# Performance work log

Measured on AMD Instinct MI355X. Metric: run time of the kernel, lower is better.

The kernel has to match this reference:

```python
import jax, jax.numpy as jnp
import numpy as np

N_E, E_DIM = 2048, 256
B, H, W = 32, 32, 32


def setup_inputs() -> dict:
    key = jax.random.key(0)
    k1, k2 = jax.random.split(key)
    z = jax.random.normal(k1, (B, E_DIM, H, W), dtype=jnp.float32)
    embedding = jax.random.normal(k2, (N_E, E_DIM), dtype=jnp.float32)
    return {"z": z, "embedding": embedding}


def reference(z, embedding):
    # z: [B, C, H, W] with C == e_dim; embedding: [n_e, e_dim]
    n_e, e_dim = embedding.shape
    b, c, h, w = z.shape
    z_nhwc = jnp.transpose(z, (0, 2, 3, 1))            # [B,H,W,C]
    z_flat = z_nhwc.reshape(-1, e_dim)                 # [L, D]
    # squared euclidean distance: ||z||^2 + ||e||^2 - 2 z.e^T
    d = (
        jnp.sum(z_flat * z_flat, axis=1, keepdims=True)
        + jnp.sum(embedding * embedding, axis=1)
        - 2.0 * jnp.einsum("ld,nd->ln", z_flat, embedding)
    )                                                  # [L, n_e]
    idx = jnp.argmin(d, axis=1)                        # [L]
    z_q = jnp.take(embedding, idx, axis=0).reshape(b, h, w, e_dim)
    # embed_ema=True -> commitment-only loss (codebook updated by EMA, not grads)
    loss = jnp.mean((jax.lax.stop_gradient(z_q) - z_nhwc) ** 2)
    # straight-through estimator
    z_q_st = z_nhwc + jax.lax.stop_gradient(z_q - z_nhwc)
    quantize = jnp.transpose(z_q_st, (0, 3, 1, 2))     # [B,C,H,W]
    # number of distinct codebook entries used (jit-safe via scatter-set)
    used = jnp.sum(jnp.zeros((n_e,), z.dtype).at[idx].set(1.0))
    index = idx.reshape(b, h, w)
    return quantize, loss, index, used
```

## Files before the change

### kernel.cpp

```cpp
#include <hip/hip_runtime.h>
#include <cfloat>

#define Dm 256
#define HW 1024
#define NE 2048
#define L_TOT 32768
#define QOFF 8388608
#define TAU 0.02f

typedef __attribute__((ext_vector_type(8))) short bf16x8;
typedef __attribute__((ext_vector_type(4))) float f32x4;
typedef const __attribute__((address_space(1))) unsigned int* as1_u32p;
typedef __attribute__((address_space(3))) unsigned int* as3_u32p;

#define GLL(gp, lp) __builtin_amdgcn_global_load_lds((as1_u32p)(gp), (as3_u32p)(lp), 16, 0, 0)

__device__ __forceinline__ unsigned short f2bf(float x) {
    unsigned u = __float_as_uint(x);
    unsigned r = (u + 0x7fffu + ((u >> 16) & 1u)) >> 16;
    return (unsigned short)r;
}
__device__ __forceinline__ float bf2f(unsigned short h) {
    return __uint_as_float(((unsigned)h) << 16);
}

__global__ void k_enorm(const float* __restrict__ emb, float* __restrict__ enorm) {
    int w = threadIdx.x >> 6, lane = threadIdx.x & 63;
    int n = blockIdx.x * 4 + w;
    const float4 v = *reinterpret_cast<const float4*>(emb + (size_t)n * Dm + lane * 4);
    double s = (double)v.x * v.x + (double)v.y * v.y + (double)v.z * v.z + (double)v.w * v.w;
    #pragma unroll
    for (int off = 32; off; off >>= 1) s += __shfl_xor(s, off);
    if (lane == 0) enorm[n] = (float)s;
}

__global__ __launch_bounds__(256) void k_split_e_norm(
    const float* __restrict__ emb, unsigned short* __restrict__ e_hi,
    unsigned short* __restrict__ e_lo, float* __restrict__ enorm)
{
    int w = threadIdx.x >> 6, lane = threadIdx.x & 63;
    int n = blockIdx.x * 4 + w;
    const float4 v = *reinterpret_cast<const float4*>(emb + (size_t)n * Dm + lane * 4);
    float vv[4] = { v.x, v.y, v.z, v.w };
    double s = (double)v.x * v.x + (double)v.y * v.y + (double)v.z * v.z + (double)v.w * v.w;
    #pragma unroll
    for (int off = 32; off; off >>= 1) s += __shfl_xor(s, off);
    if (lane == 0) enorm[n] = (float)s;
    ushort4 h4, l4;
    unsigned short* hp = (unsigned short*)&h4;
    unsigned short* lp = (unsigned short*)&l4;
    #pragma unroll
    for (int j = 0; j < 4; ++j) {
        unsigned short h = f2bf(vv[j]);
        hp[j] = h;
        lp[j] = f2bf(vv[j] - bf2f(h));
    }
    *reinterpret_cast<ushort4*>(e_hi + (size_t)n * Dm + lane * 4) = h4;
    *reinterpret_cast<ushort4*>(e_lo + (size_t)n * Dm + lane * 4) = l4;
}

__global__ __launch_bounds__(256) void k_split_z(const float* __restrict__ z,
                                                 unsigned short* __restrict__ z_hi,
                                                 unsigned short* __restrict__ z_lo) {
    __shared__ unsigned short zh[32][260];
    __shared__ unsigned short zl[32][260];
    const int b  = blockIdx.x >> 5;
    const int p0 = (blockIdx.x & 31) * 32;
    const int t  = threadIdx.x;
    const int pp = t & 31, cb = t >> 5;
    const float* zb = z + (size_t)b * (Dm * HW) + p0 + pp;
    for (int ci = 0; ci < 32; ++ci) {
        int c = ci * 8 + cb;
        float x = zb[(size_t)c * HW];
        unsigned short h = f2bf(x);
        zh[pp][c] = h;
        zl[pp][c] = f2bf(x - bf2f(h));
    }
    __syncthreads();
    const int l0 = b * 1024 + p0;
    #pragma unroll
    for (int r = 0; r < 8; ++r) {
        int id = r * 256 + t;
        int row = id >> 6, ch = id & 63;
        *reinterpret_cast<ushort4*>(z_hi + (size_t)(l0 + row) * Dm + ch * 4) =
            *reinterpret_cast<ushort4*>(&zh[row][ch * 4]);
        *reinterpret_cast<ushort4*>(z_lo + (size_t)(l0 + row) * Dm + ch * 4) =
            *reinterpret_cast<ushort4*>(&zl[row][ch * 4]);
    }
}

__global__ __launch_bounds__(512, 4) void k_score2(
    const unsigned short* __restrict__ z_hi, const unsigned short* __restrict__ z_lo,
    const unsigned short* __restrict__ e_hi, const unsigned short* __restrict__ e_lo,
    const float* __restrict__ enorm,
    float* __restrict__ pd1, float* __restrict__ pd2, int* __restrict__ pi1)
{
    __shared__ unsigned short lds[2][2][128 * 64];

    const int t    = threadIdx.x;
    const int lane = t & 63, w = t >> 6;
    const int wm = w >> 2, wn = w & 3;
    const int c15 = lane & 15, g4 = lane >> 4;

    const int bx = blockIdx.x;
    const int wg = (bx & 7) * 64 + (bx >> 3);
    const int mi = wg >> 1, ni = wg & 1;
    const int l0 = mi * 128;
    const int nbase = ni * 1024;

    auto stage = [&](int buf, const unsigned short* As, const unsigned short* Bs,
                     int nB0, int k0) {
        #pragma unroll
        for (int r = 0; r < 2; ++r) {
            int id  = r * 512 + t;
            int row = id >> 3, ch = id & 7;
            int chg = ch ^ (row & 7);
            GLL(As + (size_t)(l0 + row) * Dm + k0 + chg * 8, &lds[buf][0][id * 8]);
            GLL(Bs + (size_t)(nB0 + row) * Dm + k0 + chg * 8, &lds[buf][1][id * 8]);
        }
    };

    float d1[4][4], d2[4][4]; int i1[4][4];
    #pragma unroll
    for (int m = 0; m < 4; ++m)
        #pragma unroll
        for (int r = 0; r < 4; ++r) { d1[m][r] = 3.4e38f; d2[m][r] = 3.4e38f; i1[m][r] = 0; }

    stage(0, z_hi, e_hi, nbase, 0);
    __syncthreads();

    int cur = 0, it = 0;
    for (int nt = 0; nt < 8; ++nt) {
        f32x4 acc[4][2];
        #pragma unroll
        for (int m = 0; m < 4; ++m)
            #pragma unroll
            for (int n = 0; n < 2; ++n) acc[m][n] = (f32x4){0.f, 0.f, 0.f, 0.f};

        for (int kt = 0; kt < 12; ++kt, ++it) {
            if (it + 1 < 96) {
                int nit = it + 1;
                int nnt = nit / 12;
                int nkt = nit - nnt * 12;
                int nterm = nkt >> 2, nkc = nkt & 3;
                const unsigned short* As = (nterm == 1) ? z_lo : z_hi;
                const unsigned short* Bs = (nterm == 2) ? e_lo : e_hi;
                stage(cur ^ 1, As, Bs, nbase + nnt * 128, nkc * 64);
            }
            const unsigned short* Ab = &lds[cur][0][0];
            const unsigned short* Bb = &lds[cur][1][0];
            #pragma unroll
            for (int ks = 0; ks < 2; ++ks) {
                bf16x8 af[4], bfr[2];
                #pragma unroll
                for (int m = 0; m < 4; ++m) {
                    int row = wm * 64 + m * 16 + c15;
                    int cc  = ks * 4 + g4;
                    af[m] = *reinterpret_cast<const bf16x8*>(
                        &Ab[row * 64 + ((cc ^ (row & 7)) << 3)]);
                }
                #pragma unroll
                for (int n = 0; n < 2; ++n) {
                    int row = wn * 32 + n * 16 + c15;
                    int cc  = ks * 4 + g4;
                    bfr[n] = *reinterpret_cast<const bf16x8*>(
                        &Bb[row * 64 + ((cc ^ (row & 7)) << 3)]);
                }
                __builtin_amdgcn_s_setprio(1);
                #pragma unroll
                for (int m = 0; m < 4; ++m)
                    #pragma unroll
                    for (int n = 0; n < 2; ++n)
                        acc[m][n] = __builtin_amdgcn_mfma_f32_16x16x32_bf16(
                            af[m], bfr[n], acc[m][n], 0, 0, 0);
                __builtin_amdgcn_s_setprio(0);
            }
            __syncthreads();
            cur ^= 1;
        }
        int n0 = nbase + nt * 128;
        #pragma unroll
        for (int n = 0; n < 2; ++n) {
            int ng = n0 + wn * 32 + n * 16 + c15;
            float en = enorm[ng];
            #pragma unroll
            for (int m = 0; m < 4; ++m)
                #pragma unroll
                for (int r = 0; r < 4; ++r) {
                    float s = fmaf(-2.f, acc[m][n][r], en);
                    if (s < d1[m][r]) { d2[m][r] = d1[m][r]; d1[m][r] = s; i1[m][r] = ng; }
                    else if (s < d2[m][r]) d2[m][r] = s;
                }
        }
    }

    #pragma unroll
    for (int off = 1; off <= 8; off <<= 1) {
        #pragma unroll
        for (int m = 0; m < 4; ++m)
            #pragma unroll
            for (int r = 0; r < 4; ++r) {
                float od1 = __shfl_xor(d1[m][r], off);
                int   oi1 = __shfl_xor(i1[m][r], off);
                float od2 = __shfl_xor(d2[m][r], off);
                float nd2 = fminf(fminf(d2[m][r], od2), fmaxf(d1[m][r], od1));
                if (od1 < d1[m][r] || (od1 == d1[m][r] && oi1 < i1[m][r])) {
                    d1[m][r] = od1; i1[m][r] = oi1;
                }
                d2[m][r] = nd2;
            }
    }

    float* rs1 = (float*)&lds[0][0][0];
    float* rs2 = rs1 + 3 * 128;
    int*   ri  = (int*)(rs2 + 3 * 128);
    if (wn > 0 && c15 == 0) {
        int s = wn - 1;
        #pragma unroll
        for (int m = 0; m < 4; ++m)
            #pragma unroll
            for (int r = 0; r < 4; ++r) {
                int q = wm * 64 + m * 16 + g4 * 4 + r;
                rs1[s * 128 + q] = d1[m][r];
                rs2[s * 128 + q] = d2[m][r];
                ri [s * 128 + q] = i1[m][r];
            }
    }
    __syncthreads();
    if (wn == 0 && c15 == 0) {
        #pragma unroll
        for (int m = 0; m < 4; ++m)
            #pragma unroll
            for (int r = 0; r < 4; ++r) {
                int q = wm * 64 + m * 16 + g4 * 4 + r;
                float bd1 = d1[m][r], bd2 = d2[m][r]; int bi1 = i1[m][r];
                #pragma unroll
                for (int s = 0; s < 3; ++s) {
                    float od1 = rs1[s * 128 + q], od2 = rs2[s * 128 + q];
                    int   oi1 = ri [s * 128 + q];
                    float nd2 = fminf(fminf(bd2, od2), fmaxf(bd1, od1));
                    if (od1 < bd1 || (od1 == bd1 && oi1 < bi1)) { bd1 = od1; bi1 = oi1; }
                    bd2 = nd2;
                }
                int gq = l0 + q;
                pd1[ni * L_TOT + gq] = bd1;
                pd2[ni * L_TOT + gq] = bd2;
                pi1[ni * L_TOT + gq] = bi1;
            }
    }
}

__global__ __launch_bounds__(256) void k_merge(
    const float* __restrict__ pd1, const float* __restrict__ pd2,
    const int* __restrict__ pi1, int* __restrict__ ws_idx,
    float* __restrict__ out_idxf, float* __restrict__ used,
    int* __restrict__ flag_cnt, int* __restrict__ flag_list)
{
    int gq = blockIdx.x * 256 + threadIdx.x;
    float d1 = pd1[gq], d2 = pd2[gq]; int i1 = pi1[gq];
    #pragma unroll
    for (int s = 1; s < 2; ++s) {
        float od1 = pd1[s * L_TOT + gq], od2 = pd2[s * L_TOT + gq];
        int   oi1 = pi1[s * L_TOT + gq];
        float nd2 = fminf(fminf(d2, od2), fmaxf(d1, od1));
        if (od1 < d1 || (od1 == d1 && oi1 < i1)) { d1 = od1; i1 = oi1; }
        d2 = nd2;
    }
    ws_idx[gq] = i1;
    out_idxf[gq] = (float)i1;
    if (d2 - d1 < TAU) {
        int pos = atomicAdd(flag_cnt, 1);
        flag_list[pos] = gq;
    } else {
        used[i1] = 1.0f;
    }
}

#define BM 64
#define BN 128
#define BK 64
__global__ __launch_bounds__(256, 2) void k_argmin_f32(
    const float* __restrict__ z, const float* __restrict__ emb,
    const float* __restrict__ enorm, int* __restrict__ ws_idx,
    float* __restrict__ out_idxf, float* __restrict__ used,
    int* __restrict__ flag_cnt, int* __restrict__ flag_list)
{
    __shared__ float zl[BK][BM];
    __shared__ float el[BK][BN + 4];
    __shared__ float rd1[4][64];
    __shared__ int   ri1[4][64];
    __shared__ float rd2[4][64];

    const int t  = threadIdx.x;
    const int tq = t & 15;
    const int tn = t >> 4;
    const int l0 = blockIdx.x * BM;
    const int b  = l0 >> 10, p0 = l0 & 1023;
    const float* zb = z + (size_t)b * (Dm * HW) + p0;

    float d1[4], d2[4]; int i1[4];
    #pragma unroll
    for (int i = 0; i < 4; ++i) { d1[i] = FLT_MAX; d2[i] = FLT_MAX; i1[i] = 0; }

    for (int nt = 0; nt < NE / BN; ++nt) {
        const int n0 = nt * BN;
        float acc[4][8];
        #pragma unroll
        for (int i = 0; i < 4; ++i)
            #pragma unroll
            for (int j = 0; j < 8; ++j) acc[i][j] = 0.f;

        for (int kc = 0; kc < Dm / BK; ++kc) {
            __syncthreads();
            #pragma unroll
            for (int r = 0; r < 4; ++r) {
                int f = r * 256 + t;
                int kk = f >> 4, q4 = (f & 15) << 2;
                float4 v = *reinterpret_cast<const float4*>(zb + (size_t)(kc * BK + kk) * HW + q4);
                *reinterpret_cast<float4*>(&zl[kk][q4]) = v;
            }
            #pragma unroll
            for (int r = 0; r < 8; ++r) {
                int f = r * 256 + t;
                int n = f >> 4, k4 = (f & 15) << 2;
                float4 v = *reinterpret_cast<const float4*>(emb + (size_t)(n0 + n) * Dm + kc * BK + k4);
                el[k4 + 0][n] = v.x; el[k4 + 1][n] = v.y;
                el[k4 + 2][n] = v.z; el[k4 + 3][n] = v.w;
            }
            __syncthreads();
            #pragma unroll 4
            for (int kk = 0; kk < BK; ++kk) {
                float4 zf = *reinterpret_cast<const float4*>(&zl[kk][tq << 2]);
                float4 e0 = *reinterpret_cast<const float4*>(&el[kk][tn << 3]);
                float4 e1 = *reinterpret_cast<const float4*>(&el[kk][(tn << 3) + 4]);
                float zr[4] = { zf.x, zf.y, zf.z, zf.w };
                float er[8] = { e0.x, e0.y, e0.z, e0.w, e1.x, e1.y, e1.z, e1.w };
                #pragma unroll
                for (int i = 0; i < 4; ++i)
                    #pragma unroll
                    for (int j = 0; j < 8; ++j)
                        acc[i][j] = fmaf(zr[i], er[j], acc[i][j]);
            }
        }
        #pragma unroll
        for (int j = 0; j < 8; ++j) {
            int ng = n0 + (tn << 3) + j;
            float en = enorm[ng];
            #pragma unroll
            for (int i = 0; i < 4; ++i) {
                float s = fmaf(-2.f, acc[i][j], en);
                if (s < d1[i]) { d2[i] = d1[i]; d1[i] = s; i1[i] = ng; }
                else if (s < d2[i]) d2[i] = s;
            }
        }
    }
    #pragma unroll
    for (int off = 16; off <= 32; off <<= 1) {
        #pragma unroll
        for (int i = 0; i < 4; ++i) {
            float od1 = __shfl_xor(d1[i], off);
            int   oi1 = __shfl_xor(i1[i], off);
            float od2 = __shfl_xor(d2[i], off);
            float nd2 = fminf(fminf(d2[i], od2), fmaxf(d1[i], od1));
            bool take = (od1 < d1[i]) || (od1 == d1[i] && oi1 < i1[i]);
            if (take) { d1[i] = od1; i1[i] = oi1; }
            d2[i] = nd2;
        }
    }
    int w = t >> 6;
    if ((t & 63) < 16) {
        #pragma unroll
        for (int i = 0; i < 4; ++i) {
            rd1[w][(tq << 2) + i] = d1[i];
            ri1[w][(tq << 2) + i] = i1[i];
            rd2[w][(tq << 2) + i] = d2[i];
        }
    }
    __syncthreads();
    if (t < 64) {
        float bd1 = rd1[0][t]; int bi1 = ri1[0][t]; float bd2 = rd2[0][t];
        #pragma unroll
        for (int ww = 1; ww < 4; ++ww) {
            float od1 = rd1[ww][t]; int oi1 = ri1[ww][t]; float od2 = rd2[ww][t];
            float nd2 = fminf(fminf(bd2, od2), fmaxf(bd1, od1));
            if (od1 < bd1 || (od1 == bd1 && oi1 < bi1)) { bd1 = od1; bi1 = oi1; }
            bd2 = nd2;
        }
        int l = l0 + t;
        ws_idx[l] = bi1;
        out_idxf[l] = (float)bi1;
        if (bd2 - bd1 < TAU) {
            int pos = atomicAdd(flag_cnt, 1);
            flag_list[pos] = l;
        } else {
            used[bi1] = 1.0f;
        }
    }
}

__global__ void k_refine(const float* __restrict__ z, const float* __restrict__ emb,
                         const int* __restrict__ flag_cnt, const int* __restrict__ flag_list,
                         int* __restrict__ ws_idx, float* __restrict__ out_idxf,
                         float* __restrict__ used)
{
    __shared__ float zrow[Dm];
    __shared__ double sd[256];
    __shared__ int    si[256];
    int nf = *flag_cnt;
    for (int fi = blockIdx.x; fi < nf; fi += gridDim.x) {
        int l = flag_list[fi];
        int b = l >> 10, p = l & 1023;
        const float* zq = z + (size_t)b * (Dm * HW) + p;
        __syncthreads();
        for (int c = threadIdx.x; c < Dm; c += blockDim.x) zrow[c] = zq[(size_t)c * HW];
        __syncthreads();
        double bd = DBL_MAX; int bi = 0;
        for (int nb = 0; nb < NE / 256; ++nb) {
            int n = nb * 256 + threadIdx.x;
            const float* er = emb + (size_t)n * Dm;
            double dt0 = 0.0, dt1 = 0.0, dt2 = 0.0, dt3 = 0.0;
            double nm0 = 0.0, nm1 = 0.0, nm2 = 0.0, nm3 = 0.0;
            for (int c = 0; c < Dm; c += 4) {
                double e0 = er[c], e1 = er[c + 1], e2 = er[c + 2], e3 = er[c + 3];
                dt0 += e0 * (double)zrow[c];     nm0 += e0 * e0;
                dt1 += e1 * (double)zrow[c + 1]; nm1 += e1 * e1;
                dt2 += e2 * (double)zrow[c + 2]; nm2 += e2 * e2;
                dt3 += e3 * (double)zrow[c + 3]; nm3 += e3 * e3;
            }
            double s = (nm0 + nm1) + (nm2 + nm3) - 2.0 * ((dt0 + dt1) + (dt2 + dt3));
            if (s < bd) { bd = s; bi = n; }
        }
        sd[threadIdx.x] = bd; si[threadIdx.x] = bi;
        __syncthreads();
        for (int st = 128; st; st >>= 1) {
            if (threadIdx.x < (unsigned)st) {
                double od = sd[threadIdx.x + st]; int oi = si[threadIdx.x + st];
                if (od < sd[threadIdx.x] || (od == sd[threadIdx.x] && oi < si[threadIdx.x])) {
                    sd[threadIdx.x] = od; si[threadIdx.x] = oi;
                }
            }
            __syncthreads();
        }
        if (threadIdx.x == 0) {
            ws_idx[l] = si[0];
            out_idxf[l] = (float)si[0];
            used[si[0]] = 1.0f;
        }
        __syncthreads();
    }
}

__global__ __launch_bounds__(256) void k_gather(
    const float* __restrict__ z, const float* __restrict__ emb,
    const int* __restrict__ ws_idx, float* __restrict__ outq,
    float* __restrict__ partials)
{
    __shared__ int sidx[64];
    __shared__ float eldT[Dm][65];
    __shared__ float wsum[4];
    const int t = threadIdx.x;
    const int l0 = blockIdx.x * 64;
    const int b = l0 >> 10, p0 = l0 & 1023;
    if (t < 64) sidx[t] = ws_idx[l0 + t];
    __syncthreads();
    int w = t >> 6, lane = t & 63;
    for (int r = 0; r < 16; ++r) {
        int q = r * 4 + w;
        const float4 v = *reinterpret_cast<const float4*>(emb + (size_t)sidx[q] * Dm + lane * 4);
        eldT[lane * 4 + 0][q] = v.x; eldT[lane * 4 + 1][q] = v.y;
        eldT[lane * 4 + 2][q] = v.z; eldT[lane * 4 + 3][q] = v.w;
    }
    __syncthreads();
    float ls = 0.f;
    const size_t obase = (size_t)b * (Dm * HW) + p0 + lane;
    for (int it = 0; it < 64; ++it) {
        int c = w * 64 + it;
        size_t o = obase + (size_t)c * HW;
        float qv = eldT[c][lane];
        float zv = z[o];
        outq[o] = qv;
        float df = qv - zv;
        ls = fmaf(df, df, ls);
    }
    #pragma unroll
    for (int off = 32; off; off >>= 1) ls += __shfl_xor(ls, off);
    if (lane == 0) wsum[w] = ls;
    __syncthreads();
    if (t == 0) partials[blockIdx.x] = wsum[0] + wsum[1] + wsum[2] + wsum[3];
}

__global__ void k_final(const float* __restrict__ partials, const float* __restrict__ used,
                        float* __restrict__ out_loss, float* __restrict__ out_used)
{
    __shared__ float s1[256], s2[256];
    int t = threadIdx.x;
    float a = partials[t] + partials[t + 256];
    float u = 0.f;
    for (int i = t; i < NE; i += 256) u += used[i];
    s1[t] = a; s2[t] = u;
    __syncthreads();
    for (int st = 128; st; st >>= 1) {
        if (t < st) { s1[t] += s1[t + st]; s2[t] += s2[t + st]; }
        __syncthreads();
    }
    if (t == 0) { *out_loss = s1[0] / 8388608.f; *out_used = s2[0]; }
}

extern "C" void kernel_launch(void* const* d_in, const int* in_sizes, int n_in,
                              void* d_out, int out_size, void* d_ws, size_t ws_size,
                              hipStream_t stream) {
    const float* z   = (const float*)d_in[0];
    const float* emb = (const float*)d_in[1];
    float* out      = (float*)d_out;
    float* outq     = out;
    float* out_loss = out + QOFF;
    float* out_idxf = out + QOFF + 1;
    float* out_used = out + QOFF + 1 + L_TOT;

    float* ws       = (float*)d_ws;
    float* enorm    = ws;
    float* used     = ws + 2048;
    float* partials = ws + 4096;
    int*   flag_cnt = (int*)(ws + 4608);
    int*   ws_idx   = (int*)(ws + 5120);
    int*   flag_list= (int*)(ws + 5120 + L_TOT);

    unsigned short* e_hi = (unsigned short*)((char*)d_ws + 282624);
    unsigned short* e_lo = e_hi + (size_t)NE * Dm;
    unsigned short* z_hi = e_lo + (size_t)NE * Dm;
    unsigned short* z_lo = z_hi + (size_t)L_TOT * Dm;
    size_t need = 282624 + 2ull * (NE + L_TOT) * Dm * sizeof(unsigned short);

    float* pd1 = outq;
    float* pd2 = outq + 2 * L_TOT;
    int*   pi1 = (int*)(outq + 4 * L_TOT);

    hipMemsetAsync(used, 0, (size_t)(2048 + 512 + 16) * 4, stream);

    if (ws_size >= need) {
        k_split_e_norm<<<NE / 4, 256, 0, stream>>>(emb, e_hi, e_lo, enorm);
        k_split_z<<<1024, 256, 0, stream>>>(z, z_hi, z_lo);
        k_score2<<<512, 512, 0, stream>>>(z_hi, z_lo, e_hi, e_lo, enorm, pd1, pd2, pi1);
        k_merge<<<L_TOT / 256, 256, 0, stream>>>(pd1, pd2, pi1, ws_idx, out_idxf, used,
                                                 flag_cnt, flag_list);
    } else {
        k_enorm<<<NE / 4, 256, 0, stream>>>(emb, enorm);
        k_argmin_f32<<<L_TOT / BM, 256, 0, stream>>>(z, emb, enorm, ws_idx, out_idxf, used,
                                                     flag_cnt, flag_list);
    }
    k_refine<<<256, 256, 0, stream>>>(z, emb, flag_cnt, flag_list, ws_idx, out_idxf, used);
    k_gather<<<L_TOT / 64, 256, 0, stream>>>(z, emb, ws_idx, outq, partials);
    k_final <<<1, 256, 0, stream>>>(partials, used, out_loss, out_used);
}
```

Baseline: 248.9 us.

## Restructure split-bf16 score GEMM into 4-way N split with per-wave stripe partials

Replaces the 512-thread score kernel with a 256-thread version. Each block now covers 128 rows by 512 codes, using BK=32 LDS tiles and 4x4 MFMA tiles per wave, so each wave does more MFMAs per LDS fragment load. The in-block cross-wave reduction through LDS is dropped. Each wave stripe instead writes its own top-2 partials, 32 stripes per row, and the merge kernel reduces all 32. This trades the block-level sync and LDS reduction for a much larger partial write and read through global memory (96 floats per row) and more kernel blocks.

```diff
diff --git a/kernel.cpp b/kernel.cpp
--- a/kernel.cpp
+++ b/kernel.cpp
@@ -89,168 +89,138 @@
     }
 }
 
-__global__ __launch_bounds__(512, 4) void k_score2(
+__global__ __launch_bounds__(256, 4) void k_score4(
     const unsigned short* __restrict__ z_hi, const unsigned short* __restrict__ z_lo,
     const unsigned short* __restrict__ e_hi, const unsigned short* __restrict__ e_lo,
     const float* __restrict__ enorm,
     float* __restrict__ pd1, float* __restrict__ pd2, int* __restrict__ pi1)
 {
-    __shared__ unsigned short lds[2][2][128 * 64];
+    __shared__ unsigned short lds[2][2][128 * 32];
 
     const int t    = threadIdx.x;
     const int lane = t & 63, w = t >> 6;
-    const int wm = w >> 2, wn = w & 3;
+    const int wm = w >> 1, wc = w & 1;
     const int c15 = lane & 15, g4 = lane >> 4;
 
     const int bx = blockIdx.x;
-    const int wg = (bx & 7) * 64 + (bx >> 3);
-    const int mi = wg >> 1, ni = wg & 1;
+    const int wg = (bx & 7) * 128 + (bx >> 3);
+    const int mi = wg >> 2, ni = wg & 3;
     const int l0 = mi * 128;
-    const int nbase = ni * 1024;
-
-    auto stage = [&](int buf, const unsigned short* As, const unsigned short* Bs,
-                     int nB0, int k0) {
-        #pragma unroll
-        for (int r = 0; r < 2; ++r) {
-            int id  = r * 512 + t;
-            int row = id >> 3, ch = id & 7;
-            int chg = ch ^ (row & 7);
-            GLL(As + (size_t)(l0 + row) * Dm + k0 + chg * 8, &lds[buf][0][id * 8]);
-            GLL(Bs + (size_t)(nB0 + row) * Dm + k0 + chg * 8, &lds[buf][1][id * 8]);
-        }
+    const int nb0 = ni * 512;
+
+    const int srow = t >> 2;
+    const int chg  = (t & 3) ^ ((srow >> 1) & 3);
+    const size_t aoff0 = (size_t)(l0 + srow) * Dm + chg * 8;
+    const size_t aoff1 = aoff0 + 64 * Dm;
+    const size_t boff0 = (size_t)(nb0 + srow) * Dm + chg * 8;
+    const size_t boff1 = boff0 + 64 * Dm;
+
+    const unsigned short* aptr[3] = { z_hi, z_lo, z_hi };
+    const unsigned short* bptr[3] = { e_hi, e_hi, e_lo };
+
+    auto stage = [&](int buf, int term, int kc, int ntb) {
+        const int k0 = kc << 5;
+        const unsigned short* As = aptr[term];
+        const unsigned short* Bs = bptr[term];
+        GLL(As + aoff0 + k0, &lds[buf][0][t * 8]);
+        GLL(As + aoff1 + k0, &lds[buf][0][t * 8 + 2048]);
+        GLL(Bs + boff0 + ntb + k0, &lds[buf][1][t * 8]);
+        GLL(Bs + boff1 + ntb + k0, &lds[buf][1][t * 8 + 2048]);
     };
 
-    float d1[4][4], d2[4][4]; int i1[4][4];
-    #pragma unroll
-    for (int m = 0; m < 4; ++m)
-        #pragma unroll
-        for (int r = 0; r < 4; ++r) { d1[m][r] = 3.4e38f; d2[m][r] = 3.4e38f; i1[m][r] = 0; }
-
-    stage(0, z_hi, e_hi, nbase, 0);
-    __syncthreads();
-
-    int cur = 0, it = 0;
-    for (int nt = 0; nt < 8; ++nt) {
-        f32x4 acc[4][2];
+    int offA[4], offB[4];
+    #pragma unroll
+    for (int m = 0; m < 4; ++m) {
+        int row = wm * 64 + m * 16 + c15;
+        offA[m] = row * 32 + ((g4 ^ ((row >> 1) & 3)) << 3);
+    }
+    #pragma unroll
+    for (int n = 0; n < 4; ++n) {
+        int row = wc * 64 + n * 16 + c15;
+        offB[n] = row * 32 + ((g4 ^ ((row >> 1) & 3)) << 3);
+    }
+
+    stage(0, 0, 0, 0);
+    __syncthreads();
+
+    for (int nt = 0; nt < 4; ++nt) {
+        const int ntb = nt * (128 * Dm);
+        f32x4 acc[4][4];
         #pragma unroll
         for (int m = 0; m < 4; ++m)
             #pragma unroll
-            for (int n = 0; n < 2; ++n) acc[m][n] = (f32x4){0.f, 0.f, 0.f, 0.f};
-
-        for (int kt = 0; kt < 12; ++kt, ++it) {
-            if (it + 1 < 96) {
-                int nit = it + 1;
-                int nnt = nit / 12;
-                int nkt = nit - nnt * 12;
-                int nterm = nkt >> 2, nkc = nkt & 3;
-                const unsigned short* As = (nterm == 1) ? z_lo : z_hi;
-                const unsigned short* Bs = (nterm == 2) ? e_lo : e_hi;
-                stage(cur ^ 1, As, Bs, nbase + nnt * 128, nkc * 64);
-            }
-            const unsigned short* Ab = &lds[cur][0][0];
-            const unsigned short* Bb = &lds[cur][1][0];
-            #pragma unroll
-            for (int ks = 0; ks < 2; ++ks) {
-                bf16x8 af[4], bfr[2];
+            for (int n = 0; n < 4; ++n) acc[m][n] = (f32x4){0.f, 0.f, 0.f, 0.f};
+
+        #pragma unroll
+        for (int kt = 0; kt < 24; ++kt) {
+            const int buf = kt & 1;
+            if (kt < 23)      stage(buf ^ 1, (kt + 1) >> 3, (kt + 1) & 7, ntb);
+            else if (nt < 3)  stage(buf ^ 1, 0, 0, ntb + 128 * Dm);
+
+            bf16x8 af[4], bfr[4];
+            #pragma unroll
+            for (int m = 0; m < 4; ++m)
+                af[m] = *reinterpret_cast<const bf16x8*>(&lds[buf][0][offA[m]]);
+            #pragma unroll
+            for (int n = 0; n < 4; ++n)
+                bfr[n] = *reinterpret_cast<const bf16x8*>(&lds[buf][1][offB[n]]);
+
+            __builtin_amdgcn_s_setprio(1);
+            #pragma unroll
+            for (int m = 0; m < 4; ++m)
                 #pragma unroll
-                for (int m = 0; m < 4; ++m) {
-                    int row = wm * 64 + m * 16 + c15;
-                    int cc  = ks * 4 + g4;
-                    af[m] = *reinterpret_cast<const bf16x8*>(
-                        &Ab[row * 64 + ((cc ^ (row & 7)) << 3)]);
-                }
-                #pragma unroll
-                for (int n = 0; n < 2; ++n) {
-                    int row = wn * 32 + n * 16 + c15;
-                    int cc  = ks * 4 + g4;
-                    bfr[n] = *reinterpret_cast<const bf16x8*>(
-                        &Bb[row * 64 + ((cc ^ (row & 7)) << 3)]);
-                }
-                __builtin_amdgcn_s_setprio(1);
-                #pragma unroll
-                for (int m = 0; m < 4; ++m)
-                    #pragma unroll
-                    for (int n = 0; n < 2; ++n)
-                        acc[m][n] = __builtin_amdgcn_mfma_f32_16x16x32_bf16(
-                            af[m], bfr[n], acc[m][n], 0, 0, 0);
-                __builtin_amdgcn_s_setprio(0);
-            }
+                for (int n = 0; n < 4; ++n)
+                    acc[m][n] = __builtin_amdgcn_mfma_f32_16x16x32_bf16(
+                        af[m], bfr[n], acc[m][n], 0, 0, 0);
+            __builtin_amdgcn_s_setprio(0);
             __syncthreads();
-            cur ^= 1;
-        }
-        int n0 = nbase + nt * 128;
-        #pragma unroll
-        for (int n = 0; n < 2; ++n) {
-            int ng = n0 + wn * 32 + n * 16 + c15;
-            float en = enorm[ng];
-            #pragma unroll
-            for (int m = 0; m < 4; ++m)
+        }
+
+        const int stripe = (ni * 4 + nt) * 2 + wc;
+        #pragma unroll
+        for (int m = 0; m < 4; ++m) {
+            float d1[4], d2[4]; int i1[4];
+            #pragma unroll
+            for (int r = 0; r < 4; ++r) { d1[r] = 3.4e38f; d2[r] = 3.4e38f; i1[r] = 0; }
+            #pragma unroll
+            for (int n = 0; n < 4; ++n) {
+                int ng = nb0 + nt * 128 + wc * 64 + n * 16 + c15;
+                float en = enorm[ng];
                 #pragma unroll
                 for (int r = 0; r < 4; ++r) {
                     float s = fmaf(-2.f, acc[m][n][r], en);
-                    if (s < d1[m][r]) { d2[m][r] = d1[m][r]; d1[m][r] = s; i1[m][r] = ng; }
-                    else if (s < d2[m][r]) d2[m][r] = s;
+                    if (s < d1[r]) { d2[r] = d1[r]; d1[r] = s; i1[r] = ng; }
+                    else if (s < d2[r]) d2[r] = s;
                 }
-        }
-    }
-
-    #pragma unroll
-    for (int off = 1; off <= 8; off <<= 1) {
-        #pragma unroll
-        for (int m = 0; m < 4; ++m)
-            #pragma unroll
-            for (int r = 0; r < 4; ++r) {
-                float od1 = __shfl_xor(d1[m][r], off);
-                int   oi1 = __shfl_xor(i1[m][r], off);
-                float od2 = __shfl_xor(d2[m][r], off);
-                float nd2 = fminf(fminf(d2[m][r], od2), fmaxf(d1[m][r], od1));
-                if (od1 < d1[m][r] || (od1 == d1[m][r] && oi1 < i1[m][r])) {
-                    d1[m][r] = od1; i1[m][r] = oi1;
+            }
+            #pragma unroll
+            for (int off = 1; off <= 8; off <<= 1) {
+                #pragma unroll
+                for (int r = 0; r < 4; ++r) {
+                    float od1 = __shfl_xor(d1[r], off);
+                    int   oi1 = __shfl_xor(i1[r], off);
+                    float od2 = __shfl_xor(d2[r], off);
+                    float nd2 = fminf(fminf(d2[r], od2), fmaxf(d1[r], od1));
+                    if (od1 < d1[r] || (od1 == d1[r] && oi1 < i1[r])) {
+                        d1[r] = od1; i1[r] = oi1;
+                    }
+                    d2[r] = nd2;
                 }
-                d2[m][r] = nd2;
-            }
-    }
-
-    float* rs1 = (float*)&lds[0][0][0];
-    float* rs2 = rs1 + 3 * 128;
-    int*   ri  = (int*)(rs2 + 3 * 128);
-    if (wn > 0 && c15 == 0) {
-        int s = wn - 1;
-        #pragma unroll
-        for (int m = 0; m < 4; ++m)
-            #pragma unroll
-            for (int r = 0; r < 4; ++r) {
-                int q = wm * 64 + m * 16 + g4 * 4 + r;
-                rs1[s * 128 + q] = d1[m][r];
-                rs2[s * 128 + q] = d2[m][r];
-                ri [s * 128 + q] = i1[m][r];
-            }
-    }
-    __syncthreads();
-    if (wn == 0 && c15 == 0) {
-        #pragma unroll
-        for (int m = 0; m < 4; ++m)
-            #pragma unroll
-            for (int r = 0; r < 4; ++r) {
-                int q = wm * 64 + m * 16 + g4 * 4 + r;
-                float bd1 = d1[m][r], bd2 = d2[m][r]; int bi1 = i1[m][r];
+            }
+            if (c15 == 0) {
                 #pragma unroll
-                for (int s = 0; s < 3; ++s) {
-                    float od1 = rs1[s * 128 + q], od2 = rs2[s * 128 + q];
-                    int   oi1 = ri [s * 128 + q];
-                    float nd2 = fminf(fminf(bd2, od2), fmaxf(bd1, od1));
-                    if (od1 < bd1 || (od1 == bd1 && oi1 < bi1)) { bd1 = od1; bi1 = oi1; }
-                    bd2 = nd2;
+                for (int r = 0; r < 4; ++r) {
+                    int gq = l0 + wm * 64 + m * 16 + g4 * 4 + r;
+                    pd1[(size_t)stripe * L_TOT + gq] = d1[r];
+                    pd2[(size_t)stripe * L_TOT + gq] = d2[r];
+                    pi1[(size_t)stripe * L_TOT + gq] = i1[r];
                 }
-                int gq = l0 + q;
-                pd1[ni * L_TOT + gq] = bd1;
-                pd2[ni * L_TOT + gq] = bd2;
-                pi1[ni * L_TOT + gq] = bi1;
-            }
-    }
-}
-
-__global__ __launch_bounds__(256) void k_merge(
+            }
+        }
+    }
+}
+
+__global__ __launch_bounds__(256) void k_merge32(
     const float* __restrict__ pd1, const float* __restrict__ pd2,
     const int* __restrict__ pi1, int* __restrict__ ws_idx,
     float* __restrict__ out_idxf, float* __restrict__ used,
@@ -259,9 +229,9 @@
     int gq = blockIdx.x * 256 + threadIdx.x;
     float d1 = pd1[gq], d2 = pd2[gq]; int i1 = pi1[gq];
     #pragma unroll
-    for (int s = 1; s < 2; ++s) {
-        float od1 = pd1[s * L_TOT + gq], od2 = pd2[s * L_TOT + gq];
-        int   oi1 = pi1[s * L_TOT + gq];
+    for (int s = 1; s < 32; ++s) {
+        float od1 = pd1[(size_t)s * L_TOT + gq], od2 = pd2[(size_t)s * L_TOT + gq];
+        int   oi1 = pi1[(size_t)s * L_TOT + gq];
         float nd2 = fminf(fminf(d2, od2), fmaxf(d1, od1));
         if (od1 < d1 || (od1 == d1 && oi1 < i1)) { d1 = od1; i1 = oi1; }
         d2 = nd2;
@@ -532,17 +502,17 @@
     size_t need = 282624 + 2ull * (NE + L_TOT) * Dm * sizeof(unsigned short);
 
     float* pd1 = outq;
-    float* pd2 = outq + 2 * L_TOT;
-    int*   pi1 = (int*)(outq + 4 * L_TOT);
+    float* pd2 = outq + 32 * L_TOT;
+    int*   pi1 = (int*)(outq + 64 * L_TOT);
 
     hipMemsetAsync(used, 0, (size_t)(2048 + 512 + 16) * 4, stream);
 
     if (ws_size >= need) {
         k_split_e_norm<<<NE / 4, 256, 0, stream>>>(emb, e_hi, e_lo, enorm);
         k_split_z<<<1024, 256, 0, stream>>>(z, z_hi, z_lo);
-        k_score2<<<512, 512, 0, stream>>>(z_hi, z_lo, e_hi, e_lo, enorm, pd1, pd2, pi1);
-        k_merge<<<L_TOT / 256, 256, 0, stream>>>(pd1, pd2, pi1, ws_idx, out_idxf, used,
-                                                 flag_cnt, flag_list);
+        k_score4<<<1024, 256, 0, stream>>>(z_hi, z_lo, e_hi, e_lo, enorm, pd1, pd2, pi1);
+        k_merge32<<<L_TOT / 256, 256, 0, stream>>>(pd1, pd2, pi1, ws_idx, out_idxf, used,
+                                                   flag_cnt, flag_list);
     } else {
         k_enorm<<<NE / 4, 256, 0, stream>>>(emb, enorm);
         k_argmin_f32<<<L_TOT / BM, 256, 0, stream>>>(z, emb, enorm, ws_idx, out_idxf, used,
```

Measured after the change: 363.9 us. +46.2%, slower.

## Compute commitment loss from z norms and argmin scores instead of re-reading z

Applied to the files above, without the earlier changes.

The loss is rebuilt algebraically as the sum of ||z||^2 plus the best score (||e||^2 - 2 z·e) per row. The z norms are accumulated in the split_z pass and the best scores are reduced in the merge kernel. The gather kernel then only writes the quantized output and no longer reads z, which removes one full pass over the input. The trade-off is that the loss now relies on the bf16-split score values and ignores small index corrections made by k_refine, so it carries a small numerical error.

```diff
diff --git a/kernel.cpp b/kernel.cpp
--- a/kernel.cpp
+++ b/kernel.cpp
@@ -61,22 +61,31 @@
 
 __global__ __launch_bounds__(256) void k_split_z(const float* __restrict__ z,
                                                  unsigned short* __restrict__ z_hi,
-                                                 unsigned short* __restrict__ z_lo) {
+                                                 unsigned short* __restrict__ z_lo,
+                                                 float* __restrict__ zn_part) {
     __shared__ unsigned short zh[32][260];
     __shared__ unsigned short zl[32][260];
+    __shared__ double zsum[4];
     const int b  = blockIdx.x >> 5;
     const int p0 = (blockIdx.x & 31) * 32;
     const int t  = threadIdx.x;
     const int pp = t & 31, cb = t >> 5;
     const float* zb = z + (size_t)b * (Dm * HW) + p0 + pp;
+    float zs = 0.f;
     for (int ci = 0; ci < 32; ++ci) {
         int c = ci * 8 + cb;
         float x = zb[(size_t)c * HW];
+        zs = fmaf(x, x, zs);
         unsigned short h = f2bf(x);
         zh[pp][c] = h;
         zl[pp][c] = f2bf(x - bf2f(h));
     }
-    __syncthreads();
+    double d = zs;
+    #pragma unroll
+    for (int off = 32; off; off >>= 1) d += __shfl_xor(d, off);
+    if ((t & 63) == 0) zsum[t >> 6] = d;
+    __syncthreads();
+    if (t == 0) zn_part[blockIdx.x] = (float)(zsum[0] + zsum[1] + zsum[2] + zsum[3]);
     const int l0 = b * 1024 + p0;
     #pragma unroll
     for (int r = 0; r < 8; ++r) {
@@ -254,14 +263,16 @@
     const float* __restrict__ pd1, const float* __restrict__ pd2,
     const int* __restrict__ pi1, int* __restrict__ ws_idx,
     float* __restrict__ out_idxf, float* __restrict__ used,
-    int* __restrict__ flag_cnt, int* __restrict__ flag_list)
-{
-    int gq = blockIdx.x * 256 + threadIdx.x;
+    int* __restrict__ flag_cnt, int* __restrict__ flag_list,
+    float* __restrict__ d1_part)
+{
+    __shared__ float sdl[256];
+    int tt = threadIdx.x;
+    int gq = blockIdx.x * 256 + tt;
     float d1 = pd1[gq], d2 = pd2[gq]; int i1 = pi1[gq];
-    #pragma unroll
-    for (int s = 1; s < 2; ++s) {
-        float od1 = pd1[s * L_TOT + gq], od2 = pd2[s * L_TOT + gq];
-        int   oi1 = pi1[s * L_TOT + gq];
+    {
+        float od1 = pd1[L_TOT + gq], od2 = pd2[L_TOT + gq];
+        int   oi1 = pi1[L_TOT + gq];
         float nd2 = fminf(fminf(d2, od2), fmaxf(d1, od1));
         if (od1 < d1 || (od1 == d1 && oi1 < i1)) { d1 = od1; i1 = oi1; }
         d2 = nd2;
@@ -274,6 +285,13 @@
     } else {
         used[i1] = 1.0f;
     }
+    sdl[tt] = d1;
+    __syncthreads();
+    for (int st = 128; st; st >>= 1) {
+        if (tt < st) sdl[tt] += sdl[tt + st];
+        __syncthreads();
+    }
+    if (tt == 0) d1_part[blockIdx.x] = sdl[0];
 }
 
 #define BM 64
@@ -451,6 +469,33 @@
 }
 
 __global__ __launch_bounds__(256) void k_gather(
+    const float* __restrict__ emb, const int* __restrict__ ws_idx,
+    float* __restrict__ outq)
+{
+    __shared__ int sidx[64];
+    __shared__ float eldT[Dm][65];
+    const int t = threadIdx.x;
+    const int l0 = blockIdx.x * 64;
+    const int b = l0 >> 10, p0 = l0 & 1023;
+    if (t < 64) sidx[t] = ws_idx[l0 + t];
+    __syncthreads();
+    int w = t >> 6, lane = t & 63;
+    for (int r = 0; r < 16; ++r) {
+        int q = r * 4 + w;
+        const float4 v = *reinterpret_cast<const float4*>(emb + (size_t)sidx[q] * Dm + lane * 4);
+        eldT[lane * 4 + 0][q] = v.x; eldT[lane * 4 + 1][q] = v.y;
+        eldT[lane * 4 + 2][q] = v.z; eldT[lane * 4 + 3][q] = v.w;
+    }
+    __syncthreads();
+    const size_t obase = (size_t)b * (Dm * HW) + p0 + lane;
+    #pragma unroll 4
+    for (int it = 0; it < 64; ++it) {
+        int c = w * 64 + it;
+        outq[obase + (size_t)c * HW] = eldT[c][lane];
+    }
+}
+
+__global__ __launch_bounds__(256) void k_gather_loss(
     const float* __restrict__ z, const float* __restrict__ emb,
     const int* __restrict__ ws_idx, float* __restrict__ outq,
     float* __restrict__ partials)
@@ -489,8 +534,29 @@
     if (t == 0) partials[blockIdx.x] = wsum[0] + wsum[1] + wsum[2] + wsum[3];
 }
 
-__global__ void k_final(const float* __restrict__ partials, const float* __restrict__ used,
+__global__ void k_final(const float* __restrict__ zn_part, const float* __restrict__ d1_part,
+                        const float* __restrict__ used,
                         float* __restrict__ out_loss, float* __restrict__ out_used)
+{
+    __shared__ double s1[256];
+    __shared__ float  s2[256];
+    int t = threadIdx.x;
+    double a = 0.0;
+    for (int i = t; i < 1024; i += 256) a += (double)zn_part[i];
+    if (t < 128) a += (double)d1_part[t];
+    float u = 0.f;
+    for (int i = t; i < NE; i += 256) u += used[i];
+    s1[t] = a; s2[t] = u;
+    __syncthreads();
+    for (int st = 128; st; st >>= 1) {
+        if (t < st) { s1[t] += s1[t + st]; s2[t] += s2[t + st]; }
+        __syncthreads();
+    }
+    if (t == 0) { *out_loss = (float)(s1[0] / 8388608.0); *out_used = s2[0]; }
+}
+
+__global__ void k_final_fb(const float* __restrict__ partials, const float* __restrict__ used,
+                           float* __restrict__ out_loss, float* __restrict__ out_used)
 {
     __shared__ float s1[256], s2[256];
     int t = threadIdx.x;
@@ -520,35 +586,39 @@
     float* ws       = (float*)d_ws;
     float* enorm    = ws;
     float* used     = ws + 2048;
-    float* partials = ws + 4096;
-    int*   flag_cnt = (int*)(ws + 4608);
-    int*   ws_idx   = (int*)(ws + 5120);
-    int*   flag_list= (int*)(ws + 5120 + L_TOT);
-
-    unsigned short* e_hi = (unsigned short*)((char*)d_ws + 282624);
+    float* zn_part  = ws + 4096;
+    float* d1_part  = ws + 5120;
+    int*   flag_cnt = (int*)(ws + 5376);
+    int*   ws_idx   = (int*)(ws + 5632);
+    int*   flag_list= (int*)(ws + 5632 + L_TOT);
+
+    unsigned short* e_hi = (unsigned short*)((char*)d_ws + 284672);
     unsigned short* e_lo = e_hi + (size_t)NE * Dm;
     unsigned short* z_hi = e_lo + (size_t)NE * Dm;
     unsigned short* z_lo = z_hi + (size_t)L_TOT * Dm;
-    size_t need = 282624 + 2ull * (NE + L_TOT) * Dm * sizeof(unsigned short);
+    size_t need = 284672 + 2ull * (NE + L_TOT) * Dm * sizeof(unsigned short);
 
     float* pd1 = outq;
     float* pd2 = outq + 2 * L_TOT;
     int*   pi1 = (int*)(outq + 4 * L_TOT);
 
-    hipMemsetAsync(used, 0, (size_t)(2048 + 512 + 16) * 4, stream);
+    hipMemsetAsync(used, 0, (size_t)3584 * 4, stream);
 
     if (ws_size >= need) {
         k_split_e_norm<<<NE / 4, 256, 0, stream>>>(emb, e_hi, e_lo, enorm);
-        k_split_z<<<1024, 256, 0, stream>>>(z, z_hi, z_lo);
+        k_split_z<<<1024, 256, 0, stream>>>(z, z_hi, z_lo, zn_part);
         k_score2<<<512, 512, 0, stream>>>(z_hi, z_lo, e_hi, e_lo, enorm, pd1, pd2, pi1);
         k_merge<<<L_TOT / 256, 256, 0, stream>>>(pd1, pd2, pi1, ws_idx, out_idxf, used,
-                                                 flag_cnt, flag_list);
+                                                 flag_cnt, flag_list, d1_part);
+        k_refine<<<256, 256, 0, stream>>>(z, emb, flag_cnt, flag_list, ws_idx, out_idxf, used);
+        k_gather<<<L_TOT / 64, 256, 0, stream>>>(emb, ws_idx, outq);
+        k_final<<<1, 256, 0, stream>>>(zn_part, d1_part, used, out_loss, out_used);
     } else {
         k_enorm<<<NE / 4, 256, 0, stream>>>(emb, enorm);
         k_argmin_f32<<<L_TOT / BM, 256, 0, stream>>>(z, emb, enorm, ws_idx, out_idxf, used,
                                                      flag_cnt, flag_list);
-    }
-    k_refine<<<256, 256, 0, stream>>>(z, emb, flag_cnt, flag_list, ws_idx, out_idxf, used);
-    k_gather<<<L_TOT / 64, 256, 0, stream>>>(z, emb, ws_idx, outq, partials);
-    k_final <<<1, 256, 0, stream>>>(partials, used, out_loss, out_used);
-}
+        k_refine<<<256, 256, 0, stream>>>(z, emb, flag_cnt, flag_list, ws_idx, out_idxf, used);
+        k_gather_loss<<<L_TOT / 64, 256, 0, stream>>>(z, emb, ws_idx, outq, zn_part);
+        k_final_fb<<<1, 256, 0, stream>>>(zn_part, used, out_loss, out_used);
+    }
+}
```

Result: no change. 248.8 us (-0.0%).
